# Kernel optimization log

Measured on AMD Instinct MI355X. Metric: run time of the kernel, lower is better.

## Reference

```python
import jax, jax.numpy as jnp
import numpy as np

N = 8192      # nodes
E = 262144    # edges per graph (avg degree 32)
D_IN = 256
HID = 64
HEADS = 2
NEG_SLOPE = 0.2  # PyG GATConv leaky_relu slope


def _self_loops(ei, n):
    loop = jnp.arange(n, dtype=ei.dtype)
    return jnp.concatenate([ei[0], loop]), jnp.concatenate([ei[1], loop])


def gat_conv(x, src, dst, W, att_src, att_dst, b, concat):
    # PyG GATConv: h=[N,H,C]; alpha=softmax_dst(leaky_relu(a_s[src]+a_d[dst]))
    n = x.shape[0]
    H, C = att_src.shape
    h = (x @ W).reshape(n, H, C)
    a_s = (h * att_src).sum(-1)           # [N,H]
    a_d = (h * att_dst).sum(-1)           # [N,H]
    e = jax.nn.leaky_relu(a_s[src] + a_d[dst], NEG_SLOPE)  # [Etot,H]
    e = e - jax.ops.segment_max(e, dst, num_segments=n)[dst]
    e = jnp.exp(e)
    denom = jax.ops.segment_sum(e, dst, num_segments=n)[dst] + 1e-16
    alpha = e / denom                     # edge softmax per target node
    msg = h[src] * alpha[:, :, None]      # [Etot,H,C]
    out = jax.ops.segment_sum(msg, dst, num_segments=n)  # [N,H,C]
    out = out.reshape(n, H * C) if concat else out.mean(axis=1)
    return out + b


def gcn_conv(x, src, dst, W, b):
    # PyG GCNConv: D^{-1/2}(A+I)D^{-1/2} X W + b (self loops already appended)
    n = x.shape[0]
    h = x @ W
    deg = jax.ops.segment_sum(jnp.ones_like(src, jnp.float32), dst, num_segments=n)
    dinv = jax.lax.rsqrt(jnp.maximum(deg, 1.0))
    norm = dinv[src] * dinv[dst]          # [Etot]
    return jax.ops.segment_sum(h[src] * norm[:, None], dst, num_segments=n) + b


def cross_attn(q_in, kv_in, Wq, bq, Wk, bk, Wv, bv, Wo, bo, num_heads):
    n, d = q_in.shape
    hd = d // num_heads
    q = (q_in @ Wq + bq).reshape(n, num_heads, hd)
    k = (kv_in @ Wk + bk).reshape(n, num_heads, hd)
    v = (kv_in @ Wv + bv).reshape(n, num_heads, hd)
    scores = jnp.einsum('qhd,khd->hqk', q, k) / np.sqrt(hd).astype(np.float32)
    attn = jax.nn.softmax(scores, axis=-1)                 # [H,N,N]
    out = jnp.einsum('hqk,khd->qhd', attn, v).reshape(n, d) @ Wo + bo
    weights = attn.mean(axis=0)[None]                      # [1,N,N] avg heads (torch default)
    return out, weights


def setup_inputs():
    key = jax.random.key(0)
    ks = jax.random.split(key, 24)
    w = lambda k, s: jax.random.normal(k, s, jnp.float32) * 0.05
    inp = {
        'x': jax.random.normal(ks[0], (N, D_IN), jnp.float32),
        'edge_index_tkg': jax.random.randint(ks[1], (2, E), 0, N, jnp.int64 if jax.config.jax_enable_x64 else jnp.int32),
        'edge_index_ekg': jax.random.randint(ks[2], (2, E), 0, N, jnp.int64 if jax.config.jax_enable_x64 else jnp.int32),
        # GAT layer 1: heads=2, concat=True
        'gat1_W': w(ks[3], (D_IN, HEADS * HID)),
        'gat1_att_src': w(ks[4], (HEADS, HID)),
        'gat1_att_dst': w(ks[5], (HEADS, HID)),
        'gat1_b': jnp.zeros((HEADS * HID,), jnp.float32),
        # GAT layer 2: heads=1, concat=False
        'gat2_W': w(ks[6], (HEADS * HID, HID)),
        'gat2_att_src': w(ks[7], (1, HID)),
        'gat2_att_dst': w(ks[8], (1, HID)),
        'gat2_b': jnp.zeros((HID,), jnp.float32),
        # GCN layers
        'gcn1_W': w(ks[9], (D_IN, HID)),
        'gcn1_b': jnp.zeros((HID,), jnp.float32),
        'gcn2_W': w(ks[10], (HID, HID)),
        'gcn2_b': jnp.zeros((HID,), jnp.float32),
        # cross attention (hidden=64, 2 heads)
        'Wq': w(ks[11], (HID, HID)), 'bq': jnp.zeros((HID,), jnp.float32),
        'Wk': w(ks[12], (HID, HID)), 'bk': jnp.zeros((HID,), jnp.float32),
        'Wv': w(ks[13], (HID, HID)), 'bv': jnp.zeros((HID,), jnp.float32),
        'Wo': w(ks[14], (HID, HID)), 'bo': jnp.zeros((HID,), jnp.float32),
        # MLP head
        'fc1_W': w(ks[15], (2 * HID, HID)), 'fc1_b': jnp.zeros((HID,), jnp.float32),
        'fc2_W': w(ks[16], (HID, 1)), 'fc2_b': jnp.zeros((1,), jnp.float32),
    }
    return inp


def reference(x, edge_index_tkg, edge_index_ekg,
              gat1_W, gat1_att_src, gat1_att_dst, gat1_b,
              gat2_W, gat2_att_src, gat2_att_dst, gat2_b,
              gcn1_W, gcn1_b, gcn2_W, gcn2_b,
              Wq, bq, Wk, bk, Wv, bv, Wo, bo,
              fc1_W, fc1_b, fc2_W, fc2_b):
    n = x.shape[0]
    src_t, dst_t = _self_loops(edge_index_tkg, n)
    src_e, dst_e = _self_loops(edge_index_ekg, n)

    h_tkg = jax.nn.elu(gat_conv(x, src_t, dst_t, gat1_W, gat1_att_src, gat1_att_dst, gat1_b, True))
    h_tkg = jax.nn.elu(gat_conv(h_tkg, src_t, dst_t, gat2_W, gat2_att_src, gat2_att_dst, gat2_b, False))

    h_ekg = jax.nn.relu(gcn_conv(x, src_e, dst_e, gcn1_W, gcn1_b))
    h_ekg = jax.nn.relu(gcn_conv(h_ekg, src_e, dst_e, gcn2_W, gcn2_b))

    h_attn, attn_weights = cross_attn(h_tkg, h_ekg, Wq, bq, Wk, bk, Wv, bv, Wo, bo, HEADS)

    h_fused = jnp.concatenate([h_tkg, h_attn], axis=1)   # [N, 2*HID]
    pred = (jax.nn.relu(h_fused @ fc1_W + fc1_b) @ fc2_W + fc2_b).squeeze(-1)
    return pred, attn_weights
```

## Files before the change

### kernel.cpp

```cpp
#include <hip/hip_runtime.h>
#include <cstdint>
#include <cstddef>

#define NN 8192
#define EE 262144
#define ET 270336

using short8  = __attribute__((ext_vector_type(8))) short;
using floatx4 = __attribute__((ext_vector_type(4))) float;

__device__ __forceinline__ unsigned short f2bf(float f) {
  unsigned int u = __float_as_uint(f);
  u += 0x7fffu + ((u >> 16) & 1u);
  return (unsigned short)(u >> 16);
}

__global__ void edge_hist2_k(const int* __restrict__ ei_t, const int* __restrict__ ei_e,
                             int* __restrict__ cnt_t, int* __restrict__ cnt_e) {
  int idx = blockIdx.x * 256 + threadIdx.x;
  int g = idx >= ET;
  int e = g ? idx - ET : idx;
  const int* ei = g ? ei_e : ei_t;
  int* cnt = g ? cnt_e : cnt_t;
  int d = (e < EE) ? ei[EE + e] : (e - EE);
  atomicAdd(&cnt[d], 1);
}

__global__ void scan2_k(int* cnt_t, int* off_t, int* cnt_e, int* off_e) {
  int* cnt = blockIdx.x ? cnt_e : cnt_t;
  int* off = blockIdx.x ? off_e : off_t;
  __shared__ int s[1024];
  int t = threadIdx.x;
  int v[8]; int base = t * 8; int sum = 0;
  #pragma unroll
  for (int j = 0; j < 8; ++j) { v[j] = cnt[base + j]; sum += v[j]; }
  s[t] = sum; __syncthreads();
  for (int o = 1; o < 1024; o <<= 1) {
    int x = (t >= o) ? s[t - o] : 0;
    __syncthreads();
    s[t] += x;
    __syncthreads();
  }
  int excl = s[t] - sum;
  #pragma unroll
  for (int j = 0; j < 8; ++j) { off[base + j] = excl; cnt[base + j] = excl; excl += v[j]; }
  if (t == 1023) off[NN] = excl;
}

__global__ void edge_scatter2_k(const int* __restrict__ ei_t, const int* __restrict__ ei_e,
                                int* __restrict__ pos_t, int* __restrict__ pos_e,
                                int* __restrict__ srcs_t, int* __restrict__ srcs_e) {
  int idx = blockIdx.x * 256 + threadIdx.x;
  int g = idx >= ET;
  int e = g ? idx - ET : idx;
  const int* ei = g ? ei_e : ei_t;
  int* pos = g ? pos_e : pos_t;
  int* srcs = g ? srcs_e : srcs_t;
  int sv, d;
  if (e < EE) { sv = ei[e]; d = ei[EE + e]; } else { sv = d = e - EE; }
  int p = atomicAdd(&pos[d], 1);
  srcs[p] = sv;
}

__device__ __forceinline__ void gemm_core(const float* __restrict__ A, int lda, int K,
                                          const float* __restrict__ Bs, int row0, int col,
                                          float acc[8]) {
  #pragma unroll
  for (int r = 0; r < 8; ++r) acc[r] = 0.f;
  for (int k = 0; k < K; k += 4) {
    float b0 = Bs[(k + 0) * 32 + col], b1 = Bs[(k + 1) * 32 + col];
    float b2 = Bs[(k + 2) * 32 + col], b3 = Bs[(k + 3) * 32 + col];
    #pragma unroll
    for (int r = 0; r < 8; ++r) {
      const float4 a4 = *(const float4*)(A + (size_t)(row0 + r) * lda + k);
      acc[r] = fmaf(a4.x, b0, acc[r]);
      acc[r] = fmaf(a4.y, b1, acc[r]);
      acc[r] = fmaf(a4.z, b2, acc[r]);
      acc[r] = fmaf(a4.w, b3, acc[r]);
    }
  }
}

__global__ __launch_bounds__(256) void mm_x_k(const float* __restrict__ x,
    const float* __restrict__ Wgat, const float* __restrict__ Wgcn,
    const float* __restrict__ as_w, const float* __restrict__ ad_w,
    float* __restrict__ h1, float* __restrict__ hg1,
    float* __restrict__ a_s1, float* __restrict__ a_d1) {
  __shared__ float Bs[256 * 32];
  const int tid = threadIdx.x, by = blockIdx.y;
  const bool gat = by < 4;
  const int NC = gat ? 128 : 64;
  const int c0 = gat ? by * 32 : (by - 4) * 32;
  const float* B = gat ? Wgat : Wgcn;
  for (int idx = tid; idx < 256 * 32; idx += 256)
    Bs[idx] = B[(idx >> 5) * NC + c0 + (idx & 31)];
  __syncthreads();
  const int row0 = blockIdx.x * 64 + (tid >> 5) * 8;
  const int col = tid & 31;
  float acc[8];
  gemm_core(x, 256, 256, Bs, row0, col, acc);
  if (gat) {
    #pragma unroll
    for (int r = 0; r < 8; ++r) h1[(size_t)(row0 + r) * 128 + c0 + col] = acc[r];
    const int head = c0 >> 6;
    const float asw = as_w[head * 64 + (c0 & 63) + col];
    const float adw = ad_w[head * 64 + (c0 & 63) + col];
    float ps[8], pd[8];
    #pragma unroll
    for (int r = 0; r < 8; ++r) { ps[r] = acc[r] * asw; pd[r] = acc[r] * adw; }
    #pragma unroll
    for (int m = 16; m >= 1; m >>= 1)
      #pragma unroll
      for (int r = 0; r < 8; ++r) { ps[r] += __shfl_xor(ps[r], m); pd[r] += __shfl_xor(pd[r], m); }
    if (col == 0) {
      #pragma unroll
      for (int r = 0; r < 8; ++r) {
        atomicAdd(&a_s1[(row0 + r) * 2 + head], ps[r]);
        atomicAdd(&a_d1[(row0 + r) * 2 + head], pd[r]);
      }
    }
  } else {
    #pragma unroll
    for (int r = 0; r < 8; ++r) hg1[(size_t)(row0 + r) * 64 + c0 + col] = acc[r];
  }
}

template<int H, int C>
__device__ __forceinline__ void gat_agg_body(const float* __restrict__ h,
    const float* __restrict__ a_s, const float* __restrict__ a_d,
    const int* __restrict__ off, const int* __restrict__ srcs,
    const float* __restrict__ bias, float* __restrict__ out, int ldout, int b) {
  constexpr int HC = H * C;
  const int tid = threadIdx.x;
  const int hd = tid / C;
  const int r0 = off[b], r1 = off[b + 1];
  __shared__ int s_src[HC];
  __shared__ float s_w[HC][H];
  float ad[H];
  #pragma unroll
  for (int hh = 0; hh < H; ++hh) ad[hh] = a_d[b * H + hh];
  float acc = 0.f, den = 0.f;
  for (int base = r0; base < r1; base += HC) {
    __syncthreads();
    int e = base + tid;
    if (e < r1) {
      int sv = srcs[e];
      s_src[tid] = sv;
      #pragma unroll
      for (int hh = 0; hh < H; ++hh) {
        float xv = a_s[sv * H + hh] + ad[hh];
        xv = xv > 0.f ? xv : 0.2f * xv;
        s_w[tid][hh] = __expf(xv);
      }
    }
    __syncthreads();
    int cnt = min(HC, r1 - base);
    for (int j = 0; j < cnt; ++j) {
      float wv = s_w[j][hd];
      den += wv;
      acc = fmaf(wv, h[(size_t)s_src[j] * HC + tid], acc);
    }
  }
  float o = acc / den + bias[tid];
  out[(size_t)b * ldout + tid] = o > 0.f ? o : (__expf(o) - 1.f);
}

template<int H, int C>
__global__ void gat_agg_k(const float* __restrict__ h, const float* __restrict__ a_s,
                          const float* __restrict__ a_d, const int* __restrict__ off,
                          const int* __restrict__ srcs, const float* __restrict__ bias,
                          float* __restrict__ out, int ldout) {
  gat_agg_body<H, C>(h, a_s, a_d, off, srcs, bias, out, ldout, blockIdx.x);
}

__global__ __launch_bounds__(128) void agg1_k(
    const float* __restrict__ h1, const float* __restrict__ a_s1, const float* __restrict__ a_d1,
    const int* __restrict__ off_t, const int* __restrict__ src_t,
    const float* __restrict__ gat1_b, float* __restrict__ g1out,
    const float* __restrict__ hg1, const int* __restrict__ off_e, const int* __restrict__ src_e,
    const float* __restrict__ gcn1_b, const float* __restrict__ gcn2_W, float* __restrict__ h2g) {
  const int tid = threadIdx.x;
  if (blockIdx.x < NN) {
    gat_agg_body<2, 64>(h1, a_s1, a_d1, off_t, src_t, gat1_b, g1out, 128, blockIdx.x);
  } else {
    const int nb = (blockIdx.x - NN) * 2;
    const int sub = tid >> 6, t = tid & 63;
    const int node = nb + sub;
    __shared__ int s_src2[2][64];
    __shared__ float s_nrm2[2][64];
    __shared__ float s_row2[2][64];
    const int r0 = off_e[node], r1 = off_e[node + 1];
    const int cA = off_e[nb + 1] - off_e[nb];
    const int cB = off_e[nb + 2] - off_e[nb + 1];
    const int trips = (max(cA, cB) + 63) >> 6;
    float dinv_b = rsqrtf((float)max(r1 - r0, 1));
    float acc = 0.f;
    for (int it = 0; it < trips; ++it) {
      __syncthreads();
      int e = r0 + it * 64 + t;
      if (e < r1) {
        int sv = src_e[e];
        s_src2[sub][t] = sv;
        int ds = off_e[sv + 1] - off_e[sv];
        s_nrm2[sub][t] = dinv_b * rsqrtf((float)max(ds, 1));
      }
      __syncthreads();
      int cnt = min(64, r1 - (r0 + it * 64));
      for (int j = 0; j < cnt; ++j)
        acc = fmaf(s_nrm2[sub][j], hg1[(size_t)s_src2[sub][j] * 64 + t], acc);
    }
    s_row2[sub][t] = fmaxf(acc + gcn1_b[t], 0.f);
    __syncthreads();
    float acc2 = 0.f;
    for (int k = 0; k < 64; ++k)
      acc2 = fmaf(s_row2[sub][k], gcn2_W[k * 64 + t], acc2);
    h2g[(size_t)node * 64 + t] = acc2;
  }
}

__global__ __launch_bounds__(256) void mm2_k(
    const float* __restrict__ g1out, const float* __restrict__ gat2_W,
    const float* __restrict__ gat2_as, const float* __restrict__ gat2_ad,
    float* __restrict__ h2, float* __restrict__ a_s2, float* __restrict__ a_d2,
    const float* __restrict__ h2g, const int* __restrict__ off_e, const int* __restrict__ src_e,
    const float* __restrict__ gcn2_b, float* __restrict__ hekg) {
  const int tid = threadIdx.x;
  if (blockIdx.x < 256) {
    __shared__ float Bs[128 * 32];
    const int bx = blockIdx.x & 127;
    const int c0 = (blockIdx.x >> 7) * 32;
    for (int idx = tid; idx < 128 * 32; idx += 256)
      Bs[idx] = gat2_W[(idx >> 5) * 64 + c0 + (idx & 31)];
    __syncthreads();
    const int row0 = bx * 64 + (tid >> 5) * 8;
    const int col = tid & 31;
    float acc[8];
    gemm_core(g1out, 128, 128, Bs, row0, col, acc);
    const float asw = gat2_as[c0 + col];
    const float adw = gat2_ad[c0 + col];
    float ps[8], pd[8];
    #pragma unroll
    for (int r = 0; r < 8; ++r) {
      h2[(size_t)(row0 + r) * 64 + c0 + col] = acc[r];
      ps[r] = acc[r] * asw; pd[r] = acc[r] * adw;
    }
    #pragma unroll
    for (int m = 16; m >= 1; m >>= 1)
      #pragma unroll
      for (int r = 0; r < 8; ++r) { ps[r] += __shfl_xor(ps[r], m); pd[r] += __shfl_xor(pd[r], m); }
    if (col == 0) {
      #pragma unroll
      for (int r = 0; r < 8; ++r) {
        atomicAdd(&a_s2[row0 + r], ps[r]);
        atomicAdd(&a_d2[row0 + r], pd[r]);
      }
    }
  } else {
    const int nb = (blockIdx.x - 256) * 4;
    const int sub = tid >> 6, t = tid & 63;
    const int node = nb + sub;
    __shared__ int s_src4[4][64];
    __shared__ float s_nrm4[4][64];
    const int r0 = off_e[node], r1 = off_e[node + 1];
    int cmax = 0;
    #pragma unroll
    for (int i = 0; i < 4; ++i) cmax = max(cmax, off_e[nb + i + 1] - off_e[nb + i]);
    const int trips = (cmax + 63) >> 6;
    float dinv_b = rsqrtf((float)max(r1 - r0, 1));
    float acc = 0.f;
    for (int it = 0; it < trips; ++it) {
      __syncthreads();
      int e = r0 + it * 64 + t;
      if (e < r1) {
        int sv = src_e[e];
        s_src4[sub][t] = sv;
        int ds = off_e[sv + 1] - off_e[sv];
        s_nrm4[sub][t] = dinv_b * rsqrtf((float)max(ds, 1));
      }
      __syncthreads();
      int cnt = min(64, r1 - (r0 + it * 64));
      for (int j = 0; j < cnt; ++j)
        acc = fmaf(s_nrm4[sub][j], h2g[(size_t)s_src4[sub][j] * 64 + t], acc);
    }
    hekg[(size_t)node * 64 + t] = fmaxf(acc + gcn2_b[t], 0.f);
  }
}

__global__ __launch_bounds__(256) void mm_qkv_k(const float* __restrict__ htkg,
    const float* __restrict__ hekg,
    const float* __restrict__ Wq, const float* __restrict__ bq,
    const float* __restrict__ Wk, const float* __restrict__ bk,
    const float* __restrict__ Wv, const float* __restrict__ bv,
    unsigned short* __restrict__ qb, unsigned short* __restrict__ kb,
    unsigned short* __restrict__ Vt) {
  __shared__ float Bs[64 * 32];
  __shared__ float Ts[32][65];
  const int tid = threadIdx.x, by = blockIdx.y;
  const int kind = by >> 1;
  const int c0 = (by & 1) * 32;
  const float* A = (kind == 0) ? htkg : hekg;
  const float* B = (kind == 0) ? Wq : (kind == 1) ? Wk : Wv;
  const float* bias = (kind == 0) ? bq : (kind == 1) ? bk : bv;
  for (int idx = tid; idx < 64 * 32; idx += 256)
    Bs[idx] = B[(idx >> 5) * 64 + c0 + (idx & 31)];
  __syncthreads();
  const int row0 = blockIdx.x * 64 + (tid >> 5) * 8;
  const int col = tid & 31;
  float acc[8];
  gemm_core(A, 64, 64, Bs, row0, col, acc);
  const float bb = bias[c0 + col];
  if (kind == 0) {
    const float SCL = 0.17677669529663687f * 1.4426950408889634f;
    #pragma unroll
    for (int r = 0; r < 8; ++r)
      qb[(size_t)(row0 + r) * 64 + c0 + col] = f2bf((acc[r] + bb) * SCL);
  } else if (kind == 1) {
    #pragma unroll
    for (int r = 0; r < 8; ++r)
      kb[(size_t)(row0 + r) * 64 + c0 + col] = f2bf(acc[r] + bb);
  } else {
    const int rl = (tid >> 5) * 8;
    #pragma unroll
    for (int r = 0; r < 8; ++r) Ts[col][rl + r] = acc[r] + bb;
    __syncthreads();
    const int c = tid >> 3, rr = (tid & 7) * 8;
    short8 pk;
    #pragma unroll
    for (int j = 0; j < 8; ++j) pk[j] = (short)f2bf(Ts[c][rr + j]);
    *(short8*)(Vt + (size_t)(c0 + c) * NN + blockIdx.x * 64 + rr) = pk;
  }
}

__global__ __launch_bounds__(256) void att_lsum_k(
    const unsigned short* __restrict__ qb, const unsigned short* __restrict__ kb,
    float* __restrict__ lsum) {
  __shared__ __align__(16) short Kbuf[2][64 * 64];
  const int tid = threadIdx.x;
  const int lane = tid & 63, wv = tid >> 6;
  const int ql = lane & 15, quad = lane >> 4;
  const int q0 = blockIdx.x * 128 + wv * 32;
  const int k0 = blockIdx.y * 1024;
  const floatx4 zf = {0.f, 0.f, 0.f, 0.f};

  short8 qf[2][2];
  #pragma unroll
  for (int qt = 0; qt < 2; ++qt)
    #pragma unroll
    for (int h = 0; h < 2; ++h)
      qf[qt][h] = *(const short8*)(qb + (size_t)(q0 + qt * 16 + ql) * 64 + h * 32 + quad * 8);

  const int sr = tid >> 3, sc = tid & 7;
  const int swc0 = (sc ^ (sr & 7)) * 8;
  const int swc1 = (sc ^ ((sr + 32) & 7)) * 8;
  short8 kr0, kr1;

  float lacc[2][2][4];
  #pragma unroll
  for (int qt = 0; qt < 2; ++qt)
    #pragma unroll
    for (int h = 0; h < 2; ++h)
      #pragma unroll
      for (int r = 0; r < 4; ++r) lacc[qt][h][r] = 0.f;

  {
    const unsigned short* src = kb + (size_t)k0 * 64;
    kr0 = *(const short8*)(src + sr * 64 + sc * 8);
    kr1 = *(const short8*)(src + (sr + 32) * 64 + sc * 8);
    *(short8*)&Kbuf[0][sr * 64 + swc0] = kr0;
    *(short8*)&Kbuf[0][(sr + 32) * 64 + swc1] = kr1;
  }
  __syncthreads();

  for (int t = 0; t < 16; ++t) {
    if (t < 15) {
      const unsigned short* src = kb + (size_t)(k0 + (t + 1) * 64) * 64;
      kr0 = *(const short8*)(src + sr * 64 + sc * 8);
      kr1 = *(const short8*)(src + (sr + 32) * 64 + sc * 8);
    }
    const short* Kc = Kbuf[t & 1];
    #pragma unroll
    for (int kt = 0; kt < 4; ++kt) {
      const int row = kt * 16 + ql;
      short8 kf[2];
      #pragma unroll
      for (int h = 0; h < 2; ++h)
        kf[h] = *(const short8*)&Kc[row * 64 + ((h * 4 + quad) ^ (row & 7)) * 8];
      #pragma unroll
      for (int qt = 0; qt < 2; ++qt)
        #pragma unroll
        for (int h = 0; h < 2; ++h) {
          floatx4 s = __builtin_amdgcn_mfma_f32_16x16x32_bf16(qf[qt][h], kf[h], zf, 0, 0, 0);
          #pragma unroll
          for (int r = 0; r < 4; ++r) lacc[qt][h][r] += __builtin_amdgcn_exp2f(s[r]);
        }
    }
    if (t < 15) {
      *(short8*)&Kbuf[(t + 1) & 1][sr * 64 + swc0] = kr0;
      *(short8*)&Kbuf[(t + 1) & 1][(sr + 32) * 64 + swc1] = kr1;
    }
    __syncthreads();
  }

  #pragma unroll
  for (int o = 8; o >= 1; o >>= 1)
    #pragma unroll
    for (int qt = 0; qt < 2; ++qt)
      #pragma unroll
      for (int h = 0; h < 2; ++h)
        #pragma unroll
        for (int r = 0; r < 4; ++r)
          lacc[qt][h][r] += __shfl_xor(lacc[qt][h][r], o, 16);
  if (ql == 0) {
    #pragma unroll
    for (int qt = 0; qt < 2; ++qt)
      #pragma unroll
      for (int h = 0; h < 2; ++h)
        #pragma unroll
        for (int r = 0; r < 4; ++r)
          atomicAdd(&lsum[(q0 + qt * 16 + quad * 4 + r) * 2 + h], lacc[qt][h][r]);
  }
}

__global__ __launch_bounds__(512, 4) void att_pv_k(
    const unsigned short* __restrict__ qb, const unsigned short* __restrict__ kb,
    const unsigned short* __restrict__ Vt, const float* __restrict__ lsum,
    float* __restrict__ attn, float* __restrict__ O) {
  __shared__ __align__(16) short Kbuf[2][64 * 64];
  __shared__ __align__(16) short Vbuf[2][64 * 64];
  __shared__ __align__(16) float Esh[8][2][16 * 36];
  const int tid = threadIdx.x;
  const int lane = tid & 63, wv = tid >> 6;
  const int ql = lane & 15, quad = lane >> 4;
  const int q0 = blockIdx.x * 128 + wv * 16;
  const int k0 = blockIdx.y * 1024;
  const floatx4 zf = {0.f, 0.f, 0.f, 0.f};

  short8 qf[2];
  #pragma unroll
  for (int h = 0; h < 2; ++h)
    qf[h] = *(const short8*)(qb + (size_t)(q0 + ql) * 64 + h * 32 + quad * 8);

  float invl[2][4];
  #pragma unroll
  for (int h = 0; h < 2; ++h)
    #pragma unroll
    for (int r = 0; r < 4; ++r)
      invl[h][r] = 1.0f / lsum[(q0 + quad * 4 + r) * 2 + h];

  const int sr = tid >> 3, sc = tid & 7;
  const int swc = (sc ^ (sr & 7)) * 8;
  short8 krg, vrg;

  floatx4 oacc[2][2];
  #pragma unroll
  for (int h = 0; h < 2; ++h)
    #pragma unroll
    for (int hf = 0; hf < 2; ++hf) oacc[h][hf] = zf;

  {
    krg = *(const short8*)(kb + (size_t)(k0 + sr) * 64 + sc * 8);
    vrg = *(const short8*)(Vt + (size_t)sr * NN + k0 + sc * 8);
    *(short8*)&Kbuf[0][sr * 64 + swc] = krg;
    *(short8*)&Vbuf[0][sr * 64 + swc] = vrg;
  }
  __syncthreads();

  for (int t = 0; t < 16; ++t) {
    if (t < 15) {
      krg = *(const short8*)(kb + (size_t)(k0 + (t + 1) * 64 + sr) * 64 + sc * 8);
      vrg = *(const short8*)(Vt + (size_t)sr * NN + k0 + (t + 1) * 64 + sc * 8);
    }
    const short* Kc = Kbuf[t & 1];
    const short* Vc = Vbuf[t & 1];
    #pragma unroll
    for (int ks = 0; ks < 2; ++ks) {
      short8 kf[2][2], vf[2][2];
      #pragma unroll
      for (int kt = 0; kt < 2; ++kt) {
        const int row = ks * 32 + kt * 16 + ql;
        #pragma unroll
        for (int h = 0; h < 2; ++h)
          kf[kt][h] = *(const short8*)&Kc[row * 64 + ((h * 4 + quad) ^ (row & 7)) * 8];
      }
      #pragma unroll
      for (int h = 0; h < 2; ++h)
        #pragma unroll
        for (int hf = 0; hf < 2; ++hf) {
          const int d = h * 32 + hf * 16 + ql;
          vf[h][hf] = *(const short8*)&Vc[d * 64 + ((ks * 4 + quad) ^ (d & 7)) * 8];
        }

      floatx4 p[2][2];
      #pragma unroll
      for (int h = 0; h < 2; ++h)
        #pragma unroll
        for (int kt = 0; kt < 2; ++kt) {
          floatx4 s = __builtin_amdgcn_mfma_f32_16x16x32_bf16(qf[h], kf[kt][h], zf, 0, 0, 0);
          #pragma unroll
          for (int r = 0; r < 4; ++r)
            p[h][kt][r] = __builtin_amdgcn_exp2f(s[r]) * invl[h][r];
        }
      #pragma unroll
      for (int kt = 0; kt < 2; ++kt)
        #pragma unroll
        for (int r = 0; r < 4; ++r)
          attn[(size_t)(q0 + quad * 4 + r) * NN + k0 + t * 64 + ks * 32 + kt * 16 + ql] =
              0.5f * (p[0][kt][r] + p[1][kt][r]);
      #pragma unroll
      for (int h = 0; h < 2; ++h)
        #pragma unroll
        for (int kt = 0; kt < 2; ++kt)
          #pragma unroll
          for (int r = 0; r < 4; ++r)
            Esh[wv][h][(quad * 4 + r) * 36 + kt * 16 + ql] = p[h][kt][r];
      #pragma unroll
      for (int h = 0; h < 2; ++h) {
        const float* ep = &Esh[wv][h][ql * 36 + quad * 8];
        float4 x0 = *(const float4*)ep;
        float4 x1 = *(const float4*)(ep + 4);
        short8 ef;
        ef[0] = (short)f2bf(x0.x); ef[1] = (short)f2bf(x0.y);
        ef[2] = (short)f2bf(x0.z); ef[3] = (short)f2bf(x0.w);
        ef[4] = (short)f2bf(x1.x); ef[5] = (short)f2bf(x1.y);
        ef[6] = (short)f2bf(x1.z); ef[7] = (short)f2bf(x1.w);
        #pragma unroll
        for (int hf = 0; hf < 2; ++hf)
          oacc[h][hf] = __builtin_amdgcn_mfma_f32_16x16x32_bf16(ef, vf[h][hf], oacc[h][hf], 0, 0, 0);
      }
    }
    if (t < 15) {
      *(short8*)&Kbuf[(t + 1) & 1][sr * 64 + swc] = krg;
      *(short8*)&Vbuf[(t + 1) & 1][sr * 64 + swc] = vrg;
    }
    __syncthreads();
  }

  #pragma unroll
  for (int h = 0; h < 2; ++h)
    #pragma unroll
    for (int hf = 0; hf < 2; ++hf)
      #pragma unroll
      for (int r = 0; r < 4; ++r)
        atomicAdd(&O[(size_t)(q0 + quad * 4 + r) * 64 + h * 32 + hf * 16 + ql], oacc[h][hf][r]);
}

__global__ __launch_bounds__(256) void tail_k(const float* __restrict__ O,
    const float* __restrict__ htkg, const float* __restrict__ Wo, const float* __restrict__ bo,
    const float* __restrict__ fc1W, const float* __restrict__ fc1b,
    const float* __restrict__ fc2W, const float* __restrict__ fc2b,
    float* __restrict__ pred) {
  __shared__ float Ws[8192];
  __shared__ float T1[2048];
  __shared__ float T2[2048];
  const int tid = threadIdx.x;
  const int col = tid & 63, rg = tid >> 6;
  const int rowbase = blockIdx.x * 32;
  for (int i = tid; i < 2048; i += 256) T1[i] = O[(size_t)rowbase * 64 + i];
  for (int i = tid; i < 4096; i += 256) Ws[i] = Wo[i];
  const float rbo = bo[col], rf1b = fc1b[col], rf2 = fc2W[col], rf2b = fc2b[0];
  __syncthreads();
  float ha[8];
  #pragma unroll
  for (int r = 0; r < 8; ++r) {
    const int row = rg * 8 + r;
    float acc = rbo;
    for (int k = 0; k < 64; ++k) acc = fmaf(T1[row * 64 + k], Ws[k * 64 + col], acc);
    ha[r] = acc;
  }
  __syncthreads();
  #pragma unroll
  for (int r = 0; r < 8; ++r) T2[(rg * 8 + r) * 64 + col] = ha[r];
  for (int i = tid; i < 2048; i += 256) T1[i] = htkg[(size_t)rowbase * 64 + i];
  for (int i = tid; i < 8192; i += 256) Ws[i] = fc1W[i];
  __syncthreads();
  #pragma unroll
  for (int r = 0; r < 8; ++r) {
    const int row = rg * 8 + r;
    float acc = rf1b;
    for (int k = 0; k < 64; ++k) acc = fmaf(T1[row * 64 + k], Ws[k * 64 + col], acc);
    for (int k = 0; k < 64; ++k) acc = fmaf(T2[row * 64 + k], Ws[(64 + k) * 64 + col], acc);
    float y = fmaxf(acc, 0.f);
    float v = y * rf2;
    #pragma unroll
    for (int m = 32; m >= 1; m >>= 1) v += __shfl_xor(v, m);
    if (col == 0) pred[rowbase + row] = v + rf2b;
  }
}

extern "C" void kernel_launch(void* const* d_in, const int* in_sizes, int n_in,
                              void* d_out, int out_size, void* d_ws, size_t ws_size,
                              hipStream_t stream) {
  (void)in_sizes; (void)n_in; (void)out_size; (void)ws_size;
  const float* x       = (const float*)d_in[0];
  const int*   ei_t    = (const int*)d_in[1];
  const int*   ei_e    = (const int*)d_in[2];
  const float* gat1_W  = (const float*)d_in[3];
  const float* gat1_as = (const float*)d_in[4];
  const float* gat1_ad = (const float*)d_in[5];
  const float* gat1_b  = (const float*)d_in[6];
  const float* gat2_W  = (const float*)d_in[7];
  const float* gat2_as = (const float*)d_in[8];
  const float* gat2_ad = (const float*)d_in[9];
  const float* gat2_b  = (const float*)d_in[10];
  const float* gcn1_W  = (const float*)d_in[11];
  const float* gcn1_b  = (const float*)d_in[12];
  const float* gcn2_W  = (const float*)d_in[13];
  const float* gcn2_b  = (const float*)d_in[14];
  const float* Wq = (const float*)d_in[15]; const float* bq = (const float*)d_in[16];
  const float* Wk = (const float*)d_in[17]; const float* bk = (const float*)d_in[18];
  const float* Wv = (const float*)d_in[19]; const float* bv = (const float*)d_in[20];
  const float* Wo = (const float*)d_in[21]; const float* bo = (const float*)d_in[22];
  const float* fc1_W = (const float*)d_in[23]; const float* fc1_b = (const float*)d_in[24];
  const float* fc2_W = (const float*)d_in[25]; const float* fc2_b = (const float*)d_in[26];

  float* out  = (float*)d_out;
  float* attn = out + NN;

  char* wsp = (char*)d_ws;
  size_t ofs = 0;
  auto take = [&](size_t bytes) -> char* {
    char* p = wsp + ofs;
    ofs = (ofs + bytes + 255) & ~(size_t)255;
    return p;
  };
  int*   pos_t = (int*)take(NN * 4);
  int*   pos_e = (int*)take(NN * 4);
  float* a_s1  = (float*)take((size_t)NN * 2 * 4);
  float* a_d1  = (float*)take((size_t)NN * 2 * 4);
  float* a_s2  = (float*)take((size_t)NN * 4);
  float* a_d2  = (float*)take((size_t)NN * 4);
  float* a_l   = (float*)take((size_t)NN * 2 * 4);
  float* Obuf  = (float*)take((size_t)NN * 64 * 4);
  const size_t zero_span = ofs;
  int* off_t = (int*)take((NN + 1) * 4);
  int* off_e = (int*)take((NN + 1) * 4);
  int* src_t = (int*)take((size_t)ET * 4);
  int* src_e = (int*)take((size_t)ET * 4);
  float* h1    = (float*)take((size_t)NN * 128 * 4);
  float* g1out = (float*)take((size_t)NN * 128 * 4);
  float* h2    = (float*)take((size_t)NN * 64 * 4);
  float* htkg  = (float*)take((size_t)NN * 64 * 4);
  float* hg1   = (float*)take((size_t)NN * 64 * 4);
  float* h2g   = (float*)take((size_t)NN * 64 * 4);
  float* hekg  = (float*)take((size_t)NN * 64 * 4);
  unsigned short* qb = (unsigned short*)take((size_t)NN * 64 * 2);
  unsigned short* kb = (unsigned short*)take((size_t)NN * 64 * 2);
  unsigned short* Vt = (unsigned short*)take((size_t)64 * NN * 2);

  hipMemsetAsync(wsp, 0, zero_span, stream);

  edge_hist2_k<<<2 * ET / 256, 256, 0, stream>>>(ei_t, ei_e, pos_t, pos_e);
  scan2_k<<<2, 1024, 0, stream>>>(pos_t, off_t, pos_e, off_e);
  edge_scatter2_k<<<2 * ET / 256, 256, 0, stream>>>(ei_t, ei_e, pos_t, pos_e, src_t, src_e);

  mm_x_k<<<dim3(128, 6), 256, 0, stream>>>(x, gat1_W, gcn1_W, gat1_as, gat1_ad,
                                           h1, hg1, a_s1, a_d1);
  agg1_k<<<NN + NN / 2, 128, 0, stream>>>(h1, a_s1, a_d1, off_t, src_t, gat1_b, g1out,
                                          hg1, off_e, src_e, gcn1_b, gcn2_W, h2g);
  mm2_k<<<256 + NN / 4, 256, 0, stream>>>(g1out, gat2_W, gat2_as, gat2_ad, h2, a_s2, a_d2,
                                          h2g, off_e, src_e, gcn2_b, hekg);
  gat_agg_k<1, 64><<<NN, 64, 0, stream>>>(h2, a_s2, a_d2, off_t, src_t, gat2_b, htkg, 64);

  mm_qkv_k<<<dim3(128, 6), 256, 0, stream>>>(htkg, hekg, Wq, bq, Wk, bk, Wv, bv, qb, kb, Vt);

  att_lsum_k<<<dim3(64, 8), 256, 0, stream>>>(qb, kb, a_l);
  att_pv_k<<<dim3(64, 8), 512, 0, stream>>>(qb, kb, Vt, a_l, attn, Obuf);

  tail_k<<<256, 256, 0, stream>>>(Obuf, htkg, Wo, bo, fc1_W, fc1_b, fc2_W, fc2_b, out);
}
```

Measured before the change: 580.7 us.

## Unroll gather loops by four with zero padding and widen lsum blocks

The neighbour-gather loops in the GAT and GCN aggregation paths are padded to a multiple of four with zero-weight dummy entries and unrolled by four, so several independent global loads can be in flight at once. The attention row-sum kernel now runs 512 threads per block, with each wave handling 16 query rows instead of 32 and each thread staging one K row instead of two. This halves per-thread registers and raises the number of waves available to hide latency. In exchange there are a few wasted gathers of row 0 and more waves sharing the LDS tile.

```diff
diff --git a/kernel.cpp b/kernel.cpp
--- a/kernel.cpp
+++ b/kernel.cpp
@@ -141,6 +141,8 @@
   for (int hh = 0; hh < H; ++hh) ad[hh] = a_d[b * H + hh];
   float acc = 0.f, den = 0.f;
   for (int base = r0; base < r1; base += HC) {
+    const int cnt = min(HC, r1 - base);
+    const int cnt4 = (cnt + 3) & ~3;
     __syncthreads();
     int e = base + tid;
     if (e < r1) {
@@ -152,13 +154,19 @@
         xv = xv > 0.f ? xv : 0.2f * xv;
         s_w[tid][hh] = __expf(xv);
       }
-    }
-    __syncthreads();
-    int cnt = min(HC, r1 - base);
-    for (int j = 0; j < cnt; ++j) {
-      float wv = s_w[j][hd];
-      den += wv;
-      acc = fmaf(wv, h[(size_t)s_src[j] * HC + tid], acc);
+    } else if (tid < cnt4) {
+      s_src[tid] = 0;
+      #pragma unroll
+      for (int hh = 0; hh < H; ++hh) s_w[tid][hh] = 0.f;
+    }
+    __syncthreads();
+    for (int j = 0; j < cnt4; j += 4) {
+      #pragma unroll
+      for (int u = 0; u < 4; ++u) {
+        float wv = s_w[j + u][hd];
+        den += wv;
+        acc = fmaf(wv, h[(size_t)s_src[j + u] * HC + tid], acc);
+      }
     }
   }
   float o = acc / den + bias[tid];
@@ -196,6 +204,8 @@
     float dinv_b = rsqrtf((float)max(r1 - r0, 1));
     float acc = 0.f;
     for (int it = 0; it < trips; ++it) {
+      const int cnt = min(64, r1 - (r0 + it * 64));
+      const int cnt4 = (cnt + 3) & ~3;
       __syncthreads();
       int e = r0 + it * 64 + t;
       if (e < r1) {
@@ -203,11 +213,16 @@
         s_src2[sub][t] = sv;
         int ds = off_e[sv + 1] - off_e[sv];
         s_nrm2[sub][t] = dinv_b * rsqrtf((float)max(ds, 1));
+      } else if (t < cnt4) {
+        s_src2[sub][t] = 0;
+        s_nrm2[sub][t] = 0.f;
       }
       __syncthreads();
-      int cnt = min(64, r1 - (r0 + it * 64));
-      for (int j = 0; j < cnt; ++j)
-        acc = fmaf(s_nrm2[sub][j], hg1[(size_t)s_src2[sub][j] * 64 + t], acc);
+      for (int j = 0; j < cnt4; j += 4) {
+        #pragma unroll
+        for (int u = 0; u < 4; ++u)
+          acc = fmaf(s_nrm2[sub][j + u], hg1[(size_t)s_src2[sub][j + u] * 64 + t], acc);
+      }
     }
     s_row2[sub][t] = fmaxf(acc + gcn1_b[t], 0.f);
     __syncthreads();
@@ -269,6 +284,8 @@
     float dinv_b = rsqrtf((float)max(r1 - r0, 1));
     float acc = 0.f;
     for (int it = 0; it < trips; ++it) {
+      const int cnt = min(64, r1 - (r0 + it * 64));
+      const int cnt4 = (cnt + 3) & ~3;
       __syncthreads();
       int e = r0 + it * 64 + t;
       if (e < r1) {
@@ -276,11 +293,16 @@
         s_src4[sub][t] = sv;
         int ds = off_e[sv + 1] - off_e[sv];
         s_nrm4[sub][t] = dinv_b * rsqrtf((float)max(ds, 1));
+      } else if (t < cnt4) {
+        s_src4[sub][t] = 0;
+        s_nrm4[sub][t] = 0.f;
       }
       __syncthreads();
-      int cnt = min(64, r1 - (r0 + it * 64));
-      for (int j = 0; j < cnt; ++j)
-        acc = fmaf(s_nrm4[sub][j], h2g[(size_t)s_src4[sub][j] * 64 + t], acc);
+      for (int j = 0; j < cnt4; j += 4) {
+        #pragma unroll
+        for (int u = 0; u < 4; ++u)
+          acc = fmaf(s_nrm4[sub][j + u], h2g[(size_t)s_src4[sub][j + u] * 64 + t], acc);
+      }
     }
     hekg[(size_t)node * 64 + t] = fmaxf(acc + gcn2_b[t], 0.f);
   }
@@ -331,52 +353,41 @@
   }
 }
 
-__global__ __launch_bounds__(256) void att_lsum_k(
+__global__ __launch_bounds__(512) void att_lsum_k(
     const unsigned short* __restrict__ qb, const unsigned short* __restrict__ kb,
     float* __restrict__ lsum) {
   __shared__ __align__(16) short Kbuf[2][64 * 64];
   const int tid = threadIdx.x;
   const int lane = tid & 63, wv = tid >> 6;
   const int ql = lane & 15, quad = lane >> 4;
-  const int q0 = blockIdx.x * 128 + wv * 32;
+  const int q0 = blockIdx.x * 128 + wv * 16;
   const int k0 = blockIdx.y * 1024;
   const floatx4 zf = {0.f, 0.f, 0.f, 0.f};
 
-  short8 qf[2][2];
-  #pragma unroll
-  for (int qt = 0; qt < 2; ++qt)
-    #pragma unroll
-    for (int h = 0; h < 2; ++h)
-      qf[qt][h] = *(const short8*)(qb + (size_t)(q0 + qt * 16 + ql) * 64 + h * 32 + quad * 8);
+  short8 qf[2];
+  #pragma unroll
+  for (int h = 0; h < 2; ++h)
+    qf[h] = *(const short8*)(qb + (size_t)(q0 + ql) * 64 + h * 32 + quad * 8);
 
   const int sr = tid >> 3, sc = tid & 7;
-  const int swc0 = (sc ^ (sr & 7)) * 8;
-  const int swc1 = (sc ^ ((sr + 32) & 7)) * 8;
-  short8 kr0, kr1;
-
-  float lacc[2][2][4];
-  #pragma unroll
-  for (int qt = 0; qt < 2; ++qt)
-    #pragma unroll
-    for (int h = 0; h < 2; ++h)
-      #pragma unroll
-      for (int r = 0; r < 4; ++r) lacc[qt][h][r] = 0.f;
+  const int swc = (sc ^ (sr & 7)) * 8;
+  short8 krg;
+
+  float lacc[2][4];
+  #pragma unroll
+  for (int h = 0; h < 2; ++h)
+    #pragma unroll
+    for (int r = 0; r < 4; ++r) lacc[h][r] = 0.f;
 
   {
-    const unsigned short* src = kb + (size_t)k0 * 64;
-    kr0 = *(const short8*)(src + sr * 64 + sc * 8);
-    kr1 = *(const short8*)(src + (sr + 32) * 64 + sc * 8);
-    *(short8*)&Kbuf[0][sr * 64 + swc0] = kr0;
-    *(short8*)&Kbuf[0][(sr + 32) * 64 + swc1] = kr1;
+    krg = *(const short8*)(kb + (size_t)(k0 + sr) * 64 + sc * 8);
+    *(short8*)&Kbuf[0][sr * 64 + swc] = krg;
   }
   __syncthreads();
 
   for (int t = 0; t < 16; ++t) {
-    if (t < 15) {
-      const unsigned short* src = kb + (size_t)(k0 + (t + 1) * 64) * 64;
-      kr0 = *(const short8*)(src + sr * 64 + sc * 8);
-      kr1 = *(const short8*)(src + (sr + 32) * 64 + sc * 8);
-    }
+    if (t < 15)
+      krg = *(const short8*)(kb + (size_t)(k0 + (t + 1) * 64 + sr) * 64 + sc * 8);
     const short* Kc = Kbuf[t & 1];
     #pragma unroll
     for (int kt = 0; kt < 4; ++kt) {
@@ -386,38 +397,30 @@
       for (int h = 0; h < 2; ++h)
         kf[h] = *(const short8*)&Kc[row * 64 + ((h * 4 + quad) ^ (row & 7)) * 8];
       #pragma unroll
-      for (int qt = 0; qt < 2; ++qt)
-        #pragma unroll
-        for (int h = 0; h < 2; ++h) {
-          floatx4 s = __builtin_amdgcn_mfma_f32_16x16x32_bf16(qf[qt][h], kf[h], zf, 0, 0, 0);
-          #pragma unroll
-          for (int r = 0; r < 4; ++r) lacc[qt][h][r] += __builtin_amdgcn_exp2f(s[r]);
-        }
-    }
-    if (t < 15) {
-      *(short8*)&Kbuf[(t + 1) & 1][sr * 64 + swc0] = kr0;
-      *(short8*)&Kbuf[(t + 1) & 1][(sr + 32) * 64 + swc1] = kr1;
-    }
+      for (int h = 0; h < 2; ++h) {
+        floatx4 s = __builtin_amdgcn_mfma_f32_16x16x32_bf16(qf[h], kf[h], zf, 0, 0, 0);
+        #pragma unroll
+        for (int r = 0; r < 4; ++r) lacc[h][r] += __builtin_amdgcn_exp2f(s[r]);
+      }
+    }
+    if (t < 15)
+      *(short8*)&Kbuf[(t + 1) & 1][sr * 64 + swc] = krg;
     __syncthreads();
   }
 
   #pragma unroll
   for (int o = 8; o >= 1; o >>= 1)
     #pragma unroll
-    for (int qt = 0; qt < 2; ++qt)
-      #pragma unroll
-      for (int h = 0; h < 2; ++h)
-        #pragma unroll
-        for (int r = 0; r < 4; ++r)
-          lacc[qt][h][r] += __shfl_xor(lacc[qt][h][r], o, 16);
+    for (int h = 0; h < 2; ++h)
+      #pragma unroll
+      for (int r = 0; r < 4; ++r)
+        lacc[h][r] += __shfl_xor(lacc[h][r], o, 16);
   if (ql == 0) {
     #pragma unroll
-    for (int qt = 0; qt < 2; ++qt)
-      #pragma unroll
-      for (int h = 0; h < 2; ++h)
-        #pragma unroll
-        for (int r = 0; r < 4; ++r)
-          atomicAdd(&lsum[(q0 + qt * 16 + quad * 4 + r) * 2 + h], lacc[qt][h][r]);
+    for (int h = 0; h < 2; ++h)
+      #pragma unroll
+      for (int r = 0; r < 4; ++r)
+        atomicAdd(&lsum[(q0 + quad * 4 + r) * 2 + h], lacc[h][r]);
   }
 }
 
@@ -663,7 +666,7 @@
 
   mm_qkv_k<<<dim3(128, 6), 256, 0, stream>>>(htkg, hekg, Wq, bq, Wk, bk, Wv, bv, qb, kb, Vt);
 
-  att_lsum_k<<<dim3(64, 8), 256, 0, stream>>>(qb, kb, a_l);
+  att_lsum_k<<<dim3(64, 8), 512, 0, stream>>>(qb, kb, a_l);
   att_pv_k<<<dim3(64, 8), 512, 0, stream>>>(qb, kb, Vt, a_l, attn, Obuf);
 
   tail_k<<<256, 256, 0, stream>>>(Obuf, htkg, Wo, bo, fc1_W, fc1_b, fc2_W, fc2_b, out);
```

New measurement: 578.4 us. No clear change (-0.4%).
